# Kernel optimization log

Hardware: AMD Instinct MI355X
Metric: run time of the kernel (lower is better)

Reference implementation:

```python
import jax, jax.numpy as jnp
import numpy as np

D_MODEL = 1024
N_HEADS = 16
LN_EPS = 1e-6  # flax LayerNorm default

def setup_inputs() -> dict:
    key = jax.random.key(0)
    k1, k2, k3 = jax.random.split(key, 3)
    B, S = 2, 2048
    x = jax.random.normal(k1, (B, S, D_MODEL), dtype=jnp.float32)
    W_qkv = jax.random.normal(k2, (D_MODEL, 3 * D_MODEL), dtype=jnp.float32) / np.sqrt(D_MODEL)
    W_out = jax.random.normal(k3, (D_MODEL, D_MODEL), dtype=jnp.float32) / np.sqrt(D_MODEL)
    q_scale = jnp.ones((D_MODEL,), dtype=jnp.float32)
    k_scale = jnp.ones((D_MODEL,), dtype=jnp.float32)
    return {"x": x, "W_qkv": W_qkv, "q_scale": q_scale, "k_scale": k_scale, "W_out": W_out}

def _layernorm(t, scale):
    mu = jnp.mean(t, axis=-1, keepdims=True)
    var = jnp.var(t, axis=-1, keepdims=True)
    return (t - mu) * jax.lax.rsqrt(var + LN_EPS) * scale

def reference(x, W_qkv, q_scale, k_scale, W_out):
    B, S, D = x.shape
    H = N_HEADS
    Hd = D // H
    # fused QKV projection (no bias)
    qkv = jnp.einsum('bsd,de->bse', x, W_qkv)
    q, k, v = jnp.split(qkv, 3, axis=-1)
    # QK-LayerNorm over full d_model (before head split), scale only
    q = _layernorm(q, q_scale)
    k = _layernorm(k, k_scale)
    # split heads: [b, s, h, hd]
    q = q.reshape(B, S, H, Hd)
    k = k.reshape(B, S, H, Hd)
    v = v.reshape(B, S, H, Hd)
    # eager attention with causal mask
    scores = jnp.einsum('bshd,bthd->bhst', q / jnp.sqrt(Hd).astype(q.dtype), k)  # [b,h,s,t]
    future = jnp.triu(jnp.ones((S, S), dtype=bool), 1)  # True on strictly-future positions
    scores = jnp.where(future[None, None, :, :], jnp.finfo(scores.dtype).min, scores)
    attn = jax.nn.softmax(scores, axis=-1)
    ctx = jnp.einsum('bhst,bthd->bshd', attn, v)
    out = jnp.einsum('bsd,de->bse', ctx.reshape(B, S, D), W_out)
    return out
```

## Files before the change

kernel.cpp:

```cpp
#include <hip/hip_runtime.h>
#include <cstdint>
#include <cstddef>

typedef __attribute__((ext_vector_type(8))) short short8;
typedef __attribute__((ext_vector_type(4))) float floatx4;

__device__ __forceinline__ float bf2f(unsigned short u) {
  union { unsigned int i; float f; } c; c.i = ((unsigned int)u) << 16; return c.f;
}
__device__ __forceinline__ unsigned short f2bf(float f) {
  union { float f; unsigned int i; } c; c.f = f;
  unsigned int r = c.i + 0x7fffu + ((c.i >> 16) & 1u);
  return (unsigned short)(r >> 16);
}
__device__ __forceinline__ unsigned int fbits(float f) {
  union { float f; unsigned int i; } c; c.f = f; return c.i;
}

__device__ __forceinline__ void glds16(const unsigned short* g, unsigned short* l) {
  __builtin_amdgcn_global_load_lds((const __attribute__((address_space(1))) void*)g,
                                   (__attribute__((address_space(3))) void*)l, 16, 0, 0);
}

__device__ __forceinline__ void tr_tile(const float* __restrict__ in,
                                        unsigned short* __restrict__ out,
                                        int R, int C, int bx, int by, int tid,
                                        unsigned short (*t)[33]) {
  const int cx = tid & 31, rl = tid >> 5;
#pragma unroll
  for (int i = 0; i < 4; ++i)
    t[rl + i * 8][cx] = f2bf(in[(size_t)(by * 32 + rl + i * 8) * C + bx * 32 + cx]);
  __syncthreads();
  const int oc = by * 32 + cx;
#pragma unroll
  for (int i = 0; i < 4; ++i)
    out[(size_t)(bx * 32 + rl + i * 8) * R + oc] = t[cx][rl + i * 8];
}

__global__ __launch_bounds__(256) void k_prep(const float* __restrict__ x,
                                              const float* __restrict__ Wq,
                                              const float* __restrict__ Wo,
                                              unsigned short* __restrict__ x_bf,
                                              unsigned short* __restrict__ WTq,
                                              unsigned short* __restrict__ WTo) {
  __shared__ unsigned short t[32][33];
  const int bid = blockIdx.x, tid = threadIdx.x;
  if (bid < 3072) {
    tr_tile(Wq, WTq, 1024, 3072, bid % 96, bid / 96, tid, t);
  } else if (bid < 4096) {
    int v = bid - 3072;
    tr_tile(Wo, WTo, 1024, 1024, v & 31, v >> 5, tid, t);
  } else {
    int i = (bid - 4096) * 256 + tid;
    float4 v = ((const float4*)x)[i];
    ushort4 o = { f2bf(v.x), f2bf(v.y), f2bf(v.z), f2bf(v.w) };
    ((ushort4*)x_bf)[i] = o;
  }
}

template <int MT, bool F32OUT>
__global__ __launch_bounds__(256) void k_gemm_bt(const unsigned short* __restrict__ A,
                                                 const unsigned short* __restrict__ BT,
                                                 void* __restrict__ Cout,
                                                 int M, int N, int K) {
  constexpr int NI = MT / 32;
  __shared__ unsigned short As[MT * 32];
  __shared__ unsigned short Bs[128 * 32];
  const int bm = blockIdx.x * MT, bn = blockIdx.y * 128;
  const int tid = threadIdx.x;
  const int wave = tid >> 6, lane = tid & 63;
  const int wm = (wave & 1) * (MT / 2), wn = (wave >> 1) * 64;
  const int lrow = lane & 15, lgrp = lane >> 4;
  floatx4 acc[NI][4] = {};

  const int lr4 = lane >> 2, lc8 = (lane & 3) * 8;
  const int br0 = wave * 32;
  const unsigned short* Bg0 = BT + (size_t)(bn + br0 + lr4) * K + lc8;
  const unsigned short* Bg1 = BT + (size_t)(bn + br0 + 16 + lr4) * K + lc8;
  unsigned short* lB0 = &Bs[br0 * 32];
  unsigned short* lB1 = &Bs[(br0 + 16) * 32];
  const int ar0 = wave * (MT / 4);
  const unsigned short* Ag0 = A + (size_t)(bm + ar0 + lr4) * K + lc8;
  const unsigned short* Ag1 = A + (size_t)(bm + ar0 + 16 + lr4) * K + lc8;
  unsigned short* lA0 = &As[ar0 * 32];
  unsigned short* lA1 = &As[(ar0 + 16) * 32];

  for (int k0 = 0; k0 < K; k0 += 32) {
    glds16(Ag0 + k0, lA0);
    if (MT == 128) glds16(Ag1 + k0, lA1);
    glds16(Bg0 + k0, lB0);
    glds16(Bg1 + k0, lB1);
    __syncthreads();
    short8 a[NI], bfr[4];
#pragma unroll
    for (int i = 0; i < NI; ++i)
      a[i] = *(const short8*)&As[(wm + i * 16 + lrow) * 32 + lgrp * 8];
#pragma unroll
    for (int j = 0; j < 4; ++j)
      bfr[j] = *(const short8*)&Bs[(wn + j * 16 + lrow) * 32 + lgrp * 8];
#pragma unroll
    for (int i = 0; i < NI; ++i)
#pragma unroll
      for (int j = 0; j < 4; ++j)
        acc[i][j] = __builtin_amdgcn_mfma_f32_16x16x32_bf16(a[i], bfr[j], acc[i][j], 0, 0, 0);
    __syncthreads();
  }
#pragma unroll
  for (int i = 0; i < NI; ++i)
#pragma unroll
    for (int j = 0; j < 4; ++j)
#pragma unroll
      for (int r = 0; r < 4; ++r) {
        int m = bm + wm + i * 16 + lgrp * 4 + r;
        int n = bn + wn + j * 16 + lrow;
        if (F32OUT)
          ((float*)Cout)[(size_t)m * N + n] = acc[i][j][r];
        else
          ((unsigned short*)Cout)[(size_t)m * N + n] = f2bf(acc[i][j][r]);
      }
}

__global__ __launch_bounds__(256) void k_lnv(const unsigned short* __restrict__ qkv,
                                             const float* __restrict__ q_scale,
                                             const float* __restrict__ k_scale,
                                             unsigned short* __restrict__ q_n,
                                             unsigned short* __restrict__ k_n,
                                             unsigned short* __restrict__ VT) {
  const int bid = blockIdx.x, tid = threadIdx.x;
  if (bid < 4096) {
    const int tok = bid;
    const int wave = tid >> 6, lane = tid & 63;
    __shared__ float red[2][4];
    const unsigned short* row = qkv + (size_t)tok * 3072;
#pragma unroll
    for (int seg = 0; seg < 2; ++seg) {
      const unsigned short* p  = row + seg * 1024;
      const float* sc = seg ? k_scale : q_scale;
      unsigned short* outp = (seg ? k_n : q_n) + (size_t)tok * 1024;
      ushort4 u = *(const ushort4*)&p[tid * 4];
      float xv[4] = { bf2f(u.x), bf2f(u.y), bf2f(u.z), bf2f(u.w) };
      float sum = xv[0] + xv[1] + xv[2] + xv[3];
      float sq  = xv[0]*xv[0] + xv[1]*xv[1] + xv[2]*xv[2] + xv[3]*xv[3];
      for (int off = 32; off; off >>= 1) {
        sum += __shfl_down(sum, off, 64);
        sq  += __shfl_down(sq,  off, 64);
      }
      if (lane == 0) { red[0][wave] = sum; red[1][wave] = sq; }
      __syncthreads();
      sum = red[0][0] + red[0][1] + red[0][2] + red[0][3];
      sq  = red[1][0] + red[1][1] + red[1][2] + red[1][3];
      __syncthreads();
      float mean = sum * (1.0f / 1024.0f);
      float var  = sq * (1.0f / 1024.0f) - mean * mean;
      float rstd = rsqrtf(var + 1e-6f);
      if (seg == 0) rstd *= 0.18033688011112042f;
      float4 su = *(const float4*)&sc[tid * 4];
      ushort4 o;
      o.x = f2bf((xv[0] - mean) * rstd * su.x);
      o.y = f2bf((xv[1] - mean) * rstd * su.y);
      o.z = f2bf((xv[2] - mean) * rstd * su.z);
      o.w = f2bf((xv[3] - mean) * rstd * su.w);
      *(ushort4*)&outp[tid * 4] = o;
    }
  } else {
    __shared__ unsigned short t[32][33];
    const int v = bid - 4096;
    const int bh = v & 31, b = bh >> 4, h = bh & 15;
    const int sy = (v >> 5) & 63, hx = v >> 11;
    const int cx = tid & 31, rl = tid >> 5;
#pragma unroll
    for (int i = 0; i < 4; ++i)
      t[rl + i * 8][cx] =
        qkv[(size_t)(b * 2048 + sy * 32 + rl + i * 8) * 3072 + 2048 + h * 64 + hx * 32 + cx];
    __syncthreads();
#pragma unroll
    for (int i = 0; i < 4; ++i)
      VT[((size_t)bh * 64 + hx * 32 + rl + i * 8) * 2048 + sy * 32 + cx] = t[cx][rl + i * 8];
  }
}

template <int TB, bool MASKED>
__device__ __forceinline__ void attn_tile(int t0, int qcol,
    const short8 qa0, const short8 qa1,
    const unsigned short* Ks, const unsigned short* Vs, unsigned short* Psw,
    floatx4 (&o)[4], float& lsum, int lrow, int lgrp) {
#pragma unroll
  for (int tb = 0; tb < TB; ++tb) {
    floatx4 st = {};
    short8 kb0 = *(const short8*)&Ks[(tb * 16 + lrow) * 72 + lgrp * 8];
    st = __builtin_amdgcn_mfma_f32_16x16x32_bf16(kb0, qa0, st, 0, 0, 0);
    short8 kb1 = *(const short8*)&Ks[(tb * 16 + lrow) * 72 + 32 + lgrp * 8];
    st = __builtin_amdgcn_mfma_f32_16x16x32_bf16(kb1, qa1, st, 0, 0, 0);
    float p0 = exp2f(st[0]), p1 = exp2f(st[1]);
    float p2 = exp2f(st[2]), p3 = exp2f(st[3]);
    if (MASKED) {
      const int tbase = t0 + tb * 16 + lgrp * 4;
      p0 = (tbase     <= qcol) ? p0 : 0.0f;
      p1 = (tbase + 1 <= qcol) ? p1 : 0.0f;
      p2 = (tbase + 2 <= qcol) ? p2 : 0.0f;
      p3 = (tbase + 3 <= qcol) ? p3 : 0.0f;
    }
    lsum += (p0 + p1) + (p2 + p3);
    uint2 pu;
    pu.x = (fbits(p0) >> 16) | (fbits(p1) & 0xFFFF0000u);
    pu.y = (fbits(p2) >> 16) | (fbits(p3) & 0xFFFF0000u);
    *(uint2*)&Psw[lrow * 136 + tb * 16 + lgrp * 4] = pu;
  }
#pragma unroll
  for (int kk = 0; kk < TB / 2; ++kk) {
    short8 pa = *(const short8*)&Psw[lrow * 136 + kk * 32 + lgrp * 8];
#pragma unroll
    for (int nb = 0; nb < 4; ++nb) {
      short8 vb = *(const short8*)&Vs[(nb * 16 + lrow) * 136 + kk * 32 + lgrp * 8];
      o[nb] = __builtin_amdgcn_mfma_f32_16x16x32_bf16(pa, vb, o[nb], 0, 0, 0);
    }
  }
}

__global__ __launch_bounds__(256) void k_flash(const unsigned short* __restrict__ q_n,
                                               const unsigned short* __restrict__ k_n,
                                               const unsigned short* __restrict__ VT,
                                               unsigned short* __restrict__ ctx) {
  const int S = 2048, D = 1024;
  const int bh = blockIdx.x, b = bh >> 4, h = bh & 15;
  const int qt = 31 - (int)blockIdx.y;
  const int q0 = qt * 64;
  const int tid = threadIdx.x, wave = tid >> 6, lane = tid & 63;
  const int lrow = lane & 15, lgrp = lane >> 4;
  __shared__ unsigned short Ks[128 * 72];
  __shared__ unsigned short Vs[64 * 136];
  __shared__ unsigned short Ps[4][16 * 136];
  unsigned short* Psw = Ps[wave];

  const unsigned short* kg = k_n + (size_t)(b * S) * D + h * 64;
  const unsigned short* vg = VT + (size_t)bh * 64 * S;
  const int ksr = tid >> 3, ksc = (tid & 7) * 8;
  const int vsr = tid >> 4, vsc = (tid & 15) * 8;

  const int q0w = q0 + wave * 16;
  const int qcol = q0w + lrow;
  const unsigned short* qp = q_n + (size_t)(b * S + qcol) * D + h * 64;
  const short8 qa0 = *(const short8*)(qp + lgrp * 8);
  const short8 qa1 = *(const short8*)(qp + 32 + lgrp * 8);
  floatx4 o[4] = {};
  float lsum = 0.0f;

  const int tend = q0 + 64;
  for (int t0 = 0; t0 < tend; t0 += 128) {
#pragma unroll
    for (int j = 0; j < 4; ++j) {
      int r = ksr + j * 32;
      *(int4*)&Ks[r * 72 + ksc] = *(const int4*)(kg + (size_t)(t0 + r) * D + ksc);
    }
#pragma unroll
    for (int j = 0; j < 4; ++j) {
      int r = vsr + j * 16;
      *(int4*)&Vs[r * 136 + vsc] = *(const int4*)(vg + (size_t)r * S + t0 + vsc);
    }
    __syncthreads();
    if (t0 + 128 <= q0)
      attn_tile<8, false>(t0, qcol, qa0, qa1, Ks, Vs, Psw, o, lsum, lrow, lgrp);
    else if (tend - t0 >= 128)
      attn_tile<8, true>(t0, qcol, qa0, qa1, Ks, Vs, Psw, o, lsum, lrow, lgrp);
    else
      attn_tile<4, true>(t0, qcol, qa0, qa1, Ks, Vs, Psw, o, lsum, lrow, lgrp);
    __syncthreads();
  }

  lsum += __shfl_xor(lsum, 16, 64);
  lsum += __shfl_xor(lsum, 32, 64);
  float inv[4];
#pragma unroll
  for (int r = 0; r < 4; ++r)
    inv[r] = 1.0f / __shfl(lsum, lgrp * 20 + r, 64);
  unsigned short* op = ctx + (size_t)(b * S + q0w) * D + h * 64;
#pragma unroll
  for (int nb = 0; nb < 4; ++nb)
#pragma unroll
    for (int r = 0; r < 4; ++r) {
      int row = lgrp * 4 + r;
      op[(size_t)row * D + nb * 16 + lrow] = f2bf(o[nb][r] * inv[r]);
    }
}

extern "C" void kernel_launch(void* const* d_in, const int* in_sizes, int n_in,
                              void* d_out, int out_size, void* d_ws, size_t ws_size,
                              hipStream_t stream) {
  const float* x       = (const float*)d_in[0];
  const float* W_qkv   = (const float*)d_in[1];
  const float* q_scale = (const float*)d_in[2];
  const float* k_scale = (const float*)d_in[3];
  const float* W_out   = (const float*)d_in[4];
  float* out = (float*)d_out;
  char* ws = (char*)d_ws;
  unsigned short* WT_qkv = (unsigned short*)(ws + 0);
  unsigned short* WT_out = (unsigned short*)(ws + 6291456);
  unsigned short* qkv    = (unsigned short*)(ws + 8388608);
  unsigned short* q_nb   = (unsigned short*)(ws + 33554432);
  unsigned short* k_nb   = (unsigned short*)(ws + 41943040);
  unsigned short* VT     = (unsigned short*)(ws + 50331648);
  unsigned short* x_bf   = (unsigned short*)(ws + 58720256);
  unsigned short* ctx    = qkv;

  k_prep<<<8192, 256, 0, stream>>>(x, W_qkv, W_out, x_bf, WT_qkv, WT_out);
  k_gemm_bt<128, false><<<dim3(32, 24), 256, 0, stream>>>(x_bf, WT_qkv, qkv, 4096, 3072, 1024);
  k_lnv<<<8192, 256, 0, stream>>>(qkv, q_scale, k_scale, q_nb, k_nb, VT);
  k_flash<<<dim3(32, 32), 256, 0, stream>>>(q_nb, k_nb, VT, ctx);
  k_gemm_bt<64, true><<<dim3(64, 8), 256, 0, stream>>>(ctx, WT_out, out, 4096, 1024, 1024);
}
```

Before: 189.0 us.

## Split attention key range across waves and reduce partial outputs in LDS

The flash attention kernel now has each wave handle all 64 query rows of the block against its own 32-key slice of each 128-key tile, instead of each wave owning 16 query rows over all keys. Per-wave partial outputs and row sums are then combined through shared memory in a reduction tree, and the normalized result is written with vectorized 16-byte stores. This drops the separate half-tile masked path and raises MFMA work per K/V fragment load. In exchange it needs 64 accumulator registers per lane, more LDS, and extra synchronization and reduction work in the epilogue. The diagonal tile now always computes the full 128 keys with masking.

```diff
diff --git a/kernel.cpp b/kernel.cpp
--- a/kernel.cpp
+++ b/kernel.cpp
@@ -179,41 +179,53 @@
   }
 }
 
-template <int TB, bool MASKED>
-__device__ __forceinline__ void attn_tile(int t0, int qcol,
-    const short8 qa0, const short8 qa1,
+
+#define KS_STRIDE 72
+#define VS_STRIDE 136
+#define PS_STRIDE 40
+
+template <bool MASKED>
+__device__ __forceinline__ void attn_step(int t0, int q0, int wave,
+    const short8 (&qa)[4][2],
     const unsigned short* Ks, const unsigned short* Vs, unsigned short* Psw,
-    floatx4 (&o)[4], float& lsum, int lrow, int lgrp) {
-#pragma unroll
-  for (int tb = 0; tb < TB; ++tb) {
-    floatx4 st = {};
-    short8 kb0 = *(const short8*)&Ks[(tb * 16 + lrow) * 72 + lgrp * 8];
-    st = __builtin_amdgcn_mfma_f32_16x16x32_bf16(kb0, qa0, st, 0, 0, 0);
-    short8 kb1 = *(const short8*)&Ks[(tb * 16 + lrow) * 72 + 32 + lgrp * 8];
-    st = __builtin_amdgcn_mfma_f32_16x16x32_bf16(kb1, qa1, st, 0, 0, 0);
-    float p0 = exp2f(st[0]), p1 = exp2f(st[1]);
-    float p2 = exp2f(st[2]), p3 = exp2f(st[3]);
-    if (MASKED) {
-      const int tbase = t0 + tb * 16 + lgrp * 4;
-      p0 = (tbase     <= qcol) ? p0 : 0.0f;
-      p1 = (tbase + 1 <= qcol) ? p1 : 0.0f;
-      p2 = (tbase + 2 <= qcol) ? p2 : 0.0f;
-      p3 = (tbase + 3 <= qcol) ? p3 : 0.0f;
+    floatx4 (&o)[4][4], float (&l)[4], int lrow, int lgrp) {
+  const int tw = t0 + wave * 32;
+#pragma unroll
+  for (int tb = 0; tb < 2; ++tb) {
+    short8 kb0 = *(const short8*)&Ks[(wave * 32 + tb * 16 + lrow) * KS_STRIDE + lgrp * 8];
+    short8 kb1 = *(const short8*)&Ks[(wave * 32 + tb * 16 + lrow) * KS_STRIDE + 32 + lgrp * 8];
+#pragma unroll
+    for (int qb = 0; qb < 4; ++qb) {
+      floatx4 st = {};
+      st = __builtin_amdgcn_mfma_f32_16x16x32_bf16(kb0, qa[qb][0], st, 0, 0, 0);
+      st = __builtin_amdgcn_mfma_f32_16x16x32_bf16(kb1, qa[qb][1], st, 0, 0, 0);
+      float p0 = exp2f(st[0]), p1 = exp2f(st[1]);
+      float p2 = exp2f(st[2]), p3 = exp2f(st[3]);
+      if (MASKED) {
+        const int qcol = q0 + qb * 16 + lrow;
+        const int tbase = tw + tb * 16 + lgrp * 4;
+        p0 = (tbase     <= qcol) ? p0 : 0.0f;
+        p1 = (tbase + 1 <= qcol) ? p1 : 0.0f;
+        p2 = (tbase + 2 <= qcol) ? p2 : 0.0f;
+        p3 = (tbase + 3 <= qcol) ? p3 : 0.0f;
+      }
+      l[qb] += (p0 + p1) + (p2 + p3);
+      uint2 pu;
+      pu.x = (fbits(p0) >> 16) | (fbits(p1) & 0xFFFF0000u);
+      pu.y = (fbits(p2) >> 16) | (fbits(p3) & 0xFFFF0000u);
+      *(uint2*)&Psw[(qb * 16 + lrow) * PS_STRIDE + tb * 16 + lgrp * 4] = pu;
     }
-    lsum += (p0 + p1) + (p2 + p3);
-    uint2 pu;
-    pu.x = (fbits(p0) >> 16) | (fbits(p1) & 0xFFFF0000u);
-    pu.y = (fbits(p2) >> 16) | (fbits(p3) & 0xFFFF0000u);
-    *(uint2*)&Psw[lrow * 136 + tb * 16 + lgrp * 4] = pu;
-  }
-#pragma unroll
-  for (int kk = 0; kk < TB / 2; ++kk) {
-    short8 pa = *(const short8*)&Psw[lrow * 136 + kk * 32 + lgrp * 8];
-#pragma unroll
-    for (int nb = 0; nb < 4; ++nb) {
-      short8 vb = *(const short8*)&Vs[(nb * 16 + lrow) * 136 + kk * 32 + lgrp * 8];
-      o[nb] = __builtin_amdgcn_mfma_f32_16x16x32_bf16(pa, vb, o[nb], 0, 0, 0);
-    }
+  }
+  short8 vb[4];
+#pragma unroll
+  for (int hb = 0; hb < 4; ++hb)
+    vb[hb] = *(const short8*)&Vs[(hb * 16 + lrow) * VS_STRIDE + wave * 32 + lgrp * 8];
+#pragma unroll
+  for (int qb = 0; qb < 4; ++qb) {
+    short8 pa = *(const short8*)&Psw[(qb * 16 + lrow) * PS_STRIDE + lgrp * 8];
+#pragma unroll
+    for (int hb = 0; hb < 4; ++hb)
+      o[qb][hb] = __builtin_amdgcn_mfma_f32_16x16x32_bf16(pa, vb[hb], o[qb][hb], 0, 0, 0);
   }
 }
 
@@ -227,60 +239,116 @@
   const int q0 = qt * 64;
   const int tid = threadIdx.x, wave = tid >> 6, lane = tid & 63;
   const int lrow = lane & 15, lgrp = lane >> 4;
-  __shared__ unsigned short Ks[128 * 72];
-  __shared__ unsigned short Vs[64 * 136];
-  __shared__ unsigned short Ps[4][16 * 136];
-  unsigned short* Psw = Ps[wave];
+
+  __shared__ __align__(16) unsigned char smem[56320];
+  unsigned short* Ks  = (unsigned short*)smem;
+  unsigned short* Vs  = (unsigned short*)(smem + 18432);
+  unsigned short* Psw = (unsigned short*)(smem + 35840) + wave * 64 * PS_STRIDE;
+  float* buf0 = (float*)smem;
+  float* buf1 = (float*)(smem + 16384);
+  float* Lbuf = (float*)(smem + 35840);
 
   const unsigned short* kg = k_n + (size_t)(b * S) * D + h * 64;
   const unsigned short* vg = VT + (size_t)bh * 64 * S;
   const int ksr = tid >> 3, ksc = (tid & 7) * 8;
   const int vsr = tid >> 4, vsc = (tid & 15) * 8;
 
-  const int q0w = q0 + wave * 16;
-  const int qcol = q0w + lrow;
-  const unsigned short* qp = q_n + (size_t)(b * S + qcol) * D + h * 64;
-  const short8 qa0 = *(const short8*)(qp + lgrp * 8);
-  const short8 qa1 = *(const short8*)(qp + 32 + lgrp * 8);
-  floatx4 o[4] = {};
-  float lsum = 0.0f;
+  short8 qa[4][2];
+#pragma unroll
+  for (int qb = 0; qb < 4; ++qb) {
+    const unsigned short* qp = q_n + (size_t)(b * S + q0 + qb * 16 + lrow) * D + h * 64;
+    qa[qb][0] = *(const short8*)(qp + lgrp * 8);
+    qa[qb][1] = *(const short8*)(qp + 32 + lgrp * 8);
+  }
+  floatx4 o[4][4] = {};
+  float l[4] = {};
 
   const int tend = q0 + 64;
   for (int t0 = 0; t0 < tend; t0 += 128) {
 #pragma unroll
     for (int j = 0; j < 4; ++j) {
       int r = ksr + j * 32;
-      *(int4*)&Ks[r * 72 + ksc] = *(const int4*)(kg + (size_t)(t0 + r) * D + ksc);
+      *(int4*)&Ks[r * KS_STRIDE + ksc] = *(const int4*)(kg + (size_t)(t0 + r) * D + ksc);
     }
 #pragma unroll
     for (int j = 0; j < 4; ++j) {
       int r = vsr + j * 16;
-      *(int4*)&Vs[r * 136 + vsc] = *(const int4*)(vg + (size_t)r * S + t0 + vsc);
+      *(int4*)&Vs[r * VS_STRIDE + vsc] = *(const int4*)(vg + (size_t)r * S + t0 + vsc);
     }
     __syncthreads();
     if (t0 + 128 <= q0)
-      attn_tile<8, false>(t0, qcol, qa0, qa1, Ks, Vs, Psw, o, lsum, lrow, lgrp);
-    else if (tend - t0 >= 128)
-      attn_tile<8, true>(t0, qcol, qa0, qa1, Ks, Vs, Psw, o, lsum, lrow, lgrp);
+      attn_step<false>(t0, q0, wave, qa, Ks, Vs, Psw, o, l, lrow, lgrp);
     else
-      attn_tile<4, true>(t0, qcol, qa0, qa1, Ks, Vs, Psw, o, lsum, lrow, lgrp);
-    __syncthreads();
-  }
-
-  lsum += __shfl_xor(lsum, 16, 64);
-  lsum += __shfl_xor(lsum, 32, 64);
-  float inv[4];
-#pragma unroll
-  for (int r = 0; r < 4; ++r)
-    inv[r] = 1.0f / __shfl(lsum, lgrp * 20 + r, 64);
-  unsigned short* op = ctx + (size_t)(b * S + q0w) * D + h * 64;
-#pragma unroll
-  for (int nb = 0; nb < 4; ++nb)
-#pragma unroll
-    for (int r = 0; r < 4; ++r) {
-      int row = lgrp * 4 + r;
-      op[(size_t)row * D + nb * 16 + lrow] = f2bf(o[nb][r] * inv[r]);
-    }
+      attn_step<true>(t0, q0, wave, qa, Ks, Vs, Psw, o, l, lrow, lgrp);
+    __syncthreads();
+  }
+
+#pragma unroll
+  for (int qb = 0; qb < 4; ++qb) {
+    l[qb] += __shfl_xor(l[qb], 16, 64);
+    l[qb] += __shfl_xor(l[qb], 32, 64);
+  }
+  if (lane < 16) {
+#pragma unroll
+    for (int qb = 0; qb < 4; ++qb)
+      Lbuf[wave * 64 + qb * 16 + lrow] = l[qb];
+  }
+  if (wave == 2 || wave == 3) {
+    float* bf = (wave == 2) ? buf0 : buf1;
+#pragma unroll
+    for (int qb = 0; qb < 4; ++qb)
+#pragma unroll
+      for (int hb = 0; hb < 4; ++hb)
+#pragma unroll
+        for (int r = 0; r < 4; ++r)
+          bf[(qb * 16 + lgrp * 4 + r) * 64 + hb * 16 + lrow] = o[qb][hb][r];
+  }
+  __syncthreads();
+  if (wave == 0 || wave == 1) {
+    float* bf = (wave == 0) ? buf0 : buf1;
+#pragma unroll
+    for (int qb = 0; qb < 4; ++qb)
+#pragma unroll
+      for (int hb = 0; hb < 4; ++hb)
+#pragma unroll
+        for (int r = 0; r < 4; ++r)
+          o[qb][hb][r] += bf[(qb * 16 + lgrp * 4 + r) * 64 + hb * 16 + lrow];
+    if (wave == 1)
+#pragma unroll
+      for (int qb = 0; qb < 4; ++qb)
+#pragma unroll
+        for (int hb = 0; hb < 4; ++hb)
+#pragma unroll
+          for (int r = 0; r < 4; ++r)
+            buf1[(qb * 16 + lgrp * 4 + r) * 64 + hb * 16 + lrow] = o[qb][hb][r];
+  }
+  __syncthreads();
+  if (wave == 0) {
+#pragma unroll
+    for (int qb = 0; qb < 4; ++qb)
+#pragma unroll
+      for (int hb = 0; hb < 4; ++hb)
+#pragma unroll
+        for (int r = 0; r < 4; ++r) {
+          float v = o[qb][hb][r] + buf1[(qb * 16 + lgrp * 4 + r) * 64 + hb * 16 + lrow];
+          buf0[(qb * 16 + lgrp * 4 + r) * 64 + hb * 16 + lrow] = v;
+        }
+  }
+  __syncthreads();
+  {
+    const int q = tid >> 2, cb = tid & 3;
+    float lq = Lbuf[q] + Lbuf[64 + q] + Lbuf[128 + q] + Lbuf[192 + q];
+    float inv = 1.0f / lq;
+    const float* src = buf0 + q * 64 + cb * 16;
+    short8 w0, w1;
+#pragma unroll
+    for (int i = 0; i < 8; ++i) ((unsigned short*)&w0)[i] = f2bf(src[i] * inv);
+#pragma unroll
+    for (int i = 0; i < 8; ++i) ((unsigned short*)&w1)[i] = f2bf(src[8 + i] * inv);
+    unsigned short* op = ctx + (size_t)(b * S + q0 + q) * D + h * 64 + cb * 16;
+    *(short8*)op = w0;
+    *(short8*)(op + 8) = w1;
+  }
 }
 
 extern "C" void kernel_launch(void* const* d_in, const int* in_sizes, int n_in,
```

After: 203.8 us. 1.08x slower.
